# Performance work log

Hardware: AMD Instinct MI355X
Metric: run time of the kernel (lower is better)

Reference implementation:

```python
import jax, jax.numpy as jnp
import numpy as np

ALPHA = 0.2          # LeakyReLU negative slope
THRESHOLD = 0.5      # adjacency threshold
NEG_INF = -9e15      # same fill value as torch source


def setup_inputs() -> dict:
    key = jax.random.key(0)
    k_in, k_adj, k_W, k_a = jax.random.split(key, 4)
    B, N, C = 32, 1024, 64
    inp = jax.random.normal(k_in, (B, N, C), dtype=jnp.float32)
    adj = jax.random.uniform(k_adj, (N, N), dtype=jnp.float32)
    # xavier_uniform with gain=1.414 (as in torch init)
    gain = 1.414
    lim_W = gain * np.sqrt(6.0 / (C + C))
    W = jax.random.uniform(k_W, (C, C), dtype=jnp.float32, minval=-lim_W, maxval=lim_W)
    lim_a = gain * np.sqrt(6.0 / (2 * C + 1))
    a = jax.random.uniform(k_a, (2 * C, 1), dtype=jnp.float32, minval=-lim_a, maxval=lim_a)
    return {"input": inp, "adj": adj, "W": W, "a": a}


def reference(input, adj, W, a):
    # h: [B, N, C]
    h = jnp.matmul(input, W)
    C = W.shape[0]
    a_src = a[:C, 0]   # applied to h_i (row / query node)
    a_dst = a[C:, 0]   # applied to h_j (col / neighbor node)
    # Algebraic decomposition of a^T [h_i || h_j]: outer-sum of two [B,N] vectors.
    s_src = jnp.matmul(h, a_src)  # [B, N]
    s_dst = jnp.matmul(h, a_dst)  # [B, N]
    e = jax.nn.leaky_relu(s_src[:, :, None] + s_dst[:, None, :], negative_slope=ALPHA)  # [B,N,N]
    mask = adj > THRESHOLD  # [N, N], broadcast over batch
    attention = jax.nn.softmax(jnp.where(mask[None, :, :], e, NEG_INF), axis=2)
    h_prime = jnp.matmul(attention, h)  # [B, N, C]
    return jax.nn.elu(h_prime)
```

## Files before the change

kernel.cpp:

```cpp
#include <hip/hip_runtime.h>
#include <math.h>

#define ALPHA 0.2f

constexpr int B = 32, N = 1024, C = 64;

typedef __attribute__((ext_vector_type(8))) short short8;
typedef __attribute__((ext_vector_type(4))) float floatx4;

static __device__ __forceinline__ unsigned f32bf(float f) {
    unsigned u = __float_as_uint(f);
    return (u + 0x7FFFu + ((u >> 16) & 1u)) >> 16;
}

__global__ __launch_bounds__(256) void gat_mask(const float* __restrict__ adj,
                                                const float* __restrict__ Wm,
                                                const float* __restrict__ a,
                                                unsigned long long* __restrict__ mask64,
                                                float* __restrict__ wa)
{
    const int lane = threadIdx.x & 63;
    const int wave = threadIdx.x >> 6;
    const int id   = blockIdx.x * 4 + wave;
    const int i    = id >> 4;
    const int jc   = id & 15;
    const float av = adj[(size_t)i * N + jc * 64 + lane];
    const unsigned long long bal = __ballot(av > 0.5f);
    if (lane == 0) mask64[i * 16 + jc] = bal;

    if (blockIdx.x == 0 && wave == 0) {
        float accs = 0.f, accd = 0.f;
#pragma unroll
        for (int c4 = 0; c4 < 16; ++c4) {
            const float4 wv = *(const float4*)&Wm[lane * 64 + c4 * 4];
            const float4 as = *(const float4*)&a[c4 * 4];
            const float4 ad = *(const float4*)&a[64 + c4 * 4];
            accs = fmaf(wv.x, as.x, fmaf(wv.y, as.y, fmaf(wv.z, as.z, fmaf(wv.w, as.w, accs))));
            accd = fmaf(wv.x, ad.x, fmaf(wv.y, ad.y, fmaf(wv.z, ad.z, fmaf(wv.w, ad.w, accd))));
        }
        wa[lane] = accs;
        wa[64 + lane] = accd;
    }
}

__global__ __launch_bounds__(256) void gat_hs(const float* __restrict__ input,
                                              const float* __restrict__ Wm,
                                              const float* __restrict__ wa,
                                              unsigned short* __restrict__ hT,
                                              float* __restrict__ ssrc,
                                              float* __restrict__ sdst)
{
    __shared__ __align__(16) float ins[64 * 68];
    __shared__ __align__(16) unsigned short hsT[64 * 72];
    __shared__ float red_s[256], red_d[256];
    __shared__ float wa_l[128];

    const int tid  = threadIdx.x;
    const int lane = tid & 63;
    const int wave = tid >> 6;
    const int row0 = blockIdx.x * 64;
    const int b    = row0 >> 10;
    const int jb   = row0 & 1023;

    float wreg[64];
#pragma unroll
    for (int k = 0; k < 64; ++k) wreg[k] = Wm[k * 64 + lane];

    const float4* gin = (const float4*)(input + (size_t)row0 * 64);
#pragma unroll
    for (int s = 0; s < 4; ++s) {
        const int id = tid + 256 * s;
        *(float4*)&ins[(id >> 4) * 68 + (id & 15) * 4] = gin[id];
    }
    if (tid < 128) wa_l[tid] = wa[tid];
    __syncthreads();

    for (int r = 0; r < 16; ++r) {
        const int row = wave * 16 + r;
        float acc = 0.f;
#pragma unroll
        for (int k4 = 0; k4 < 16; ++k4) {
            const float4 iv = *(const float4*)&ins[row * 68 + k4 * 4];
            acc = fmaf(iv.x, wreg[k4 * 4 + 0], acc);
            acc = fmaf(iv.y, wreg[k4 * 4 + 1], acc);
            acc = fmaf(iv.z, wreg[k4 * 4 + 2], acc);
            acc = fmaf(iv.w, wreg[k4 * 4 + 3], acc);
        }
        hsT[lane * 72 + row] = (unsigned short)f32bf(acc);
    }

    {
        const int r = tid & 63, kq = tid >> 6;
        float as = 0.f, ad = 0.f;
#pragma unroll
        for (int t = 0; t < 4; ++t) {
            const float4 iv = *(const float4*)&ins[r * 68 + kq * 16 + t * 4];
            const float4 ws = *(const float4*)&wa_l[kq * 16 + t * 4];
            const float4 wd = *(const float4*)&wa_l[64 + kq * 16 + t * 4];
            as = fmaf(iv.x, ws.x, fmaf(iv.y, ws.y, fmaf(iv.z, ws.z, fmaf(iv.w, ws.w, as))));
            ad = fmaf(iv.x, wd.x, fmaf(iv.y, wd.y, fmaf(iv.z, wd.z, fmaf(iv.w, wd.w, ad))));
        }
        red_s[tid] = as;
        red_d[tid] = ad;
    }
    __syncthreads();

    if (tid < 64) {
        ssrc[row0 + tid] = red_s[tid] + red_s[tid + 64] + red_s[tid + 128] + red_s[tid + 192];
        sdst[row0 + tid] = red_d[tid] + red_d[tid + 64] + red_d[tid + 128] + red_d[tid + 192];
    }

    {
        const int c = tid >> 2, part = tid & 3;
        const short8 v0 = *(const short8*)&hsT[c * 72 + part * 16];
        const short8 v1 = *(const short8*)&hsT[c * 72 + part * 16 + 8];
        const size_t g = ((size_t)(b * 64 + c)) * 1024 + jb + part * 16;
        *(short8*)&hT[g] = v0;
        *(short8*)&hT[g + 8] = v1;
    }
}

__global__ __launch_bounds__(256) void gat_attn(const unsigned short* __restrict__ hTg,
                                                const float* __restrict__ ssrc,
                                                const float* __restrict__ sdst,
                                                const unsigned char* __restrict__ maskB,
                                                float* __restrict__ out)
{
    __shared__ __align__(16) unsigned short p_u[2][32 * 64];
    __shared__ float psum_s[32];

    const int tid  = threadIdx.x;
    const int lane = tid & 63;
    const int wave = tid >> 6;
    const int b    = blockIdx.x & 31;
    const int i0   = (blockIdx.x >> 5) * 32;

    const int ii = tid >> 3;
    const int jo = tid & 7;
    const float ssq = ssrc[b * N + i0 + ii];
    const float* __restrict__ sd = sdst + b * N;
    const unsigned char* __restrict__ mrow = maskB + (size_t)(i0 + ii) * 128;

    const int n16 = lane & 15;
    const int kq  = lane >> 4;
    const int cB  = wave * 16 + n16;
    const unsigned short* __restrict__ hTb = hTg + ((size_t)b * 64 + cB) * 1024;

    const int pwoff = ii * 64 + (jo ^ (ii & 7)) * 8;
    const int sw    = (n16 & 7);
    const int ra0   = n16 * 64;
    const int ra1   = (16 + n16) * 64;
    const int ch0   = ((0 * 4 + kq) ^ sw) * 8;
    const int ch1   = ((1 * 4 + kq) ^ sw) * 8;

    floatx4 acc0 = {0.f, 0.f, 0.f, 0.f};
    floatx4 acc1 = {0.f, 0.f, 0.f, 0.f};
    float psacc = 0.f;

    auto compute_p = [&](int jt) -> short8 {
        const float4 s0 = *(const float4*)&sd[jt * 64 + jo * 8];
        const float4 s1 = *(const float4*)&sd[jt * 64 + jo * 8 + 4];
        const unsigned mb = mrow[jt * 8 + jo];
        const float ev[8] = {s0.x, s0.y, s0.z, s0.w, s1.x, s1.y, s1.z, s1.w};
        short8 r;
        float loc = 0.f;
#pragma unroll
        for (int k = 0; k < 8; ++k) {
            float t = ssq + ev[k];
            t = t > 0.f ? t : ALPHA * t;
            const float p = ((mb >> k) & 1u) ? __expf(t) : 0.f;
            loc += p;
            r[k] = (short)f32bf(p);
        }
        psacc += loc;
        return r;
    };
    auto load_B = [&](int jt, int t) -> short8 {
        return *(const short8*)&hTb[jt * 64 + t * 32 + kq * 8];
    };

    short8 pk = compute_p(0);
    short8 b0 = load_B(0, 0);
    short8 b1 = load_B(0, 1);

    for (int jt = 0; jt < 16; ++jt) {
        unsigned short* pb = p_u[jt & 1];
        *(short8*)&pb[pwoff] = pk;
        __syncthreads();

        short8 nb0 = b0, nb1 = b1, npk = pk;
        if (jt < 15) {
            nb0 = load_B(jt + 1, 0);
            nb1 = load_B(jt + 1, 1);
            npk = compute_p(jt + 1);
        }

        const short8 a00 = *(const short8*)&pb[ra0 + ch0];
        const short8 a01 = *(const short8*)&pb[ra0 + ch1];
        const short8 a10 = *(const short8*)&pb[ra1 + ch0];
        const short8 a11 = *(const short8*)&pb[ra1 + ch1];
        acc0 = __builtin_amdgcn_mfma_f32_16x16x32_bf16(a00, b0, acc0, 0, 0, 0);
        acc0 = __builtin_amdgcn_mfma_f32_16x16x32_bf16(a01, b1, acc0, 0, 0, 0);
        acc1 = __builtin_amdgcn_mfma_f32_16x16x32_bf16(a10, b0, acc1, 0, 0, 0);
        acc1 = __builtin_amdgcn_mfma_f32_16x16x32_bf16(a11, b1, acc1, 0, 0, 0);

        b0 = nb0; b1 = nb1; pk = npk;
    }

#pragma unroll
    for (int off = 1; off < 8; off <<= 1) psacc += __shfl_xor(psacc, off, 64);
    if (jo == 0) psum_s[ii] = psacc;
    __syncthreads();

#pragma unroll
    for (int it = 0; it < 2; ++it) {
        const floatx4 acc = it ? acc1 : acc0;
#pragma unroll
        for (int r = 0; r < 4; ++r) {
            const int row = it * 16 + kq * 4 + r;
            const float hp = acc[r] / psum_s[row];
            const float o  = hp > 0.f ? hp : __expf(hp) - 1.f;
            out[((size_t)(b * N + i0 + row)) * 64 + cB] = o;
        }
    }
}

extern "C" void kernel_launch(void* const* d_in, const int* in_sizes, int n_in,
                              void* d_out, int out_size, void* d_ws, size_t ws_size,
                              hipStream_t stream) {
    const float* input = (const float*)d_in[0];
    const float* adj   = (const float*)d_in[1];
    const float* Wm    = (const float*)d_in[2];
    const float* a     = (const float*)d_in[3];
    float* out = (float*)d_out;

    char* ws = (char*)d_ws;
    unsigned short* hT = (unsigned short*)ws;
    float* ssrc = (float*)(ws + 4194304);
    float* sdst = (float*)(ws + 4194304 + 131072);
    unsigned long long* mask64 = (unsigned long long*)(ws + 4194304 + 2 * 131072);
    float* wa = (float*)(ws + 4194304 + 3 * 131072);

    gat_mask<<<N * N / 64 / 4, 256, 0, stream>>>(adj, Wm, a, mask64, wa);
    gat_hs<<<B * N / 64, 256, 0, stream>>>(input, Wm, wa, hT, ssrc, sdst);
    gat_attn<<<(N / 32) * B, 256, 0, stream>>>(hT, ssrc, sdst, (const unsigned char*)mask64, out);
}
```

Measured before the change: 105.4 us.

## Fuse mask and projection kernels, use MFMA for projection, stage attention tiles via LDS

```diff
diff --git a/kernel.cpp b/kernel.cpp
--- a/kernel.cpp
+++ b/kernel.cpp
@@ -2,6 +2,7 @@
 #include <math.h>
 
 #define ALPHA 0.2f
+#define LOG2E 1.4426950408889634f
 
 constexpr int B = 32, N = 1024, C = 64;
 
@@ -13,202 +14,208 @@
     return (u + 0x7FFFu + ((u >> 16) & 1u)) >> 16;
 }
 
-__global__ __launch_bounds__(256) void gat_mask(const float* __restrict__ adj,
-                                                const float* __restrict__ Wm,
-                                                const float* __restrict__ a,
-                                                unsigned long long* __restrict__ mask64,
-                                                float* __restrict__ wa)
+static __device__ __forceinline__ void async_copy16(void* lds_base, const void* g) {
+    __builtin_amdgcn_global_load_lds(
+        (const __attribute__((address_space(1))) unsigned int*)g,
+        (__attribute__((address_space(3))) unsigned int*)lds_base, 16, 0, 0);
+}
+
+__global__ __launch_bounds__(256) void gat_pre(
+    const float* __restrict__ input, const float* __restrict__ adj,
+    const float* __restrict__ Wm, const float* __restrict__ a,
+    unsigned short* __restrict__ hT, float* __restrict__ ssrc,
+    float* __restrict__ sdst, unsigned long long* __restrict__ mask64)
 {
-    const int lane = threadIdx.x & 63;
-    const int wave = threadIdx.x >> 6;
-    const int id   = blockIdx.x * 4 + wave;
-    const int i    = id >> 4;
-    const int jc   = id & 15;
-    const float av = adj[(size_t)i * N + jc * 64 + lane];
-    const unsigned long long bal = __ballot(av > 0.5f);
-    if (lane == 0) mask64[i * 16 + jc] = bal;
-
-    if (blockIdx.x == 0 && wave == 0) {
-        float accs = 0.f, accd = 0.f;
-#pragma unroll
-        for (int c4 = 0; c4 < 16; ++c4) {
-            const float4 wv = *(const float4*)&Wm[lane * 64 + c4 * 4];
-            const float4 as = *(const float4*)&a[c4 * 4];
-            const float4 ad = *(const float4*)&a[64 + c4 * 4];
-            accs = fmaf(wv.x, as.x, fmaf(wv.y, as.y, fmaf(wv.z, as.z, fmaf(wv.w, as.w, accs))));
-            accd = fmaf(wv.x, ad.x, fmaf(wv.y, ad.y, fmaf(wv.z, ad.z, fmaf(wv.w, ad.w, accd))));
-        }
-        wa[lane] = accs;
-        wa[64 + lane] = accd;
-    }
-}
-
-__global__ __launch_bounds__(256) void gat_hs(const float* __restrict__ input,
-                                              const float* __restrict__ Wm,
-                                              const float* __restrict__ wa,
-                                              unsigned short* __restrict__ hT,
-                                              float* __restrict__ ssrc,
-                                              float* __restrict__ sdst)
+    const int tid = threadIdx.x, lane = tid & 63, wave = tid >> 6;
+
+    if (blockIdx.x >= 1024) {
+        const int mb = blockIdx.x - 1024;
+#pragma unroll
+        for (int t = 0; t < 4; ++t) {
+            const int id = mb * 16 + wave * 4 + t;
+            const int i = id >> 4, jc = id & 15;
+            const float av = adj[(size_t)i * N + jc * 64 + lane];
+            const unsigned long long bal = __ballot(av > 0.5f);
+            if (lane == 0) mask64[i * 16 + jc] = bal;
+        }
+        return;
+    }
+
+    __shared__ __align__(16) float W_l[64 * 65];
+    __shared__ __align__(16) float a_l[128];
+    __shared__ float wa_l[128];
+
+    const int row0 = blockIdx.x * 32;
+    const int b = row0 >> 10;
+    const int jloc0 = row0 & 1023;
+    const int m = lane & 15, kq = lane >> 4;
+
+#pragma unroll
+    for (int t = 0; t < 4; ++t) {
+        const int t4 = tid + t * 256;
+        const int base = t4 * 4;
+        *(float4*)&W_l[(base >> 6) * 65 + (base & 63)] = ((const float4*)Wm)[t4];
+    }
+    if (tid < 32) ((float4*)a_l)[tid] = ((const float4*)a)[tid];
+
+    float af[2][2][8];
+#pragma unroll
+    for (int at = 0; at < 2; ++at)
+#pragma unroll
+        for (int kc = 0; kc < 2; ++kc) {
+            const float* src = &input[(size_t)(row0 + at * 16 + m) * 64 + kc * 32 + kq * 8];
+            const float4 v0 = *(const float4*)src;
+            const float4 v1 = *(const float4*)(src + 4);
+            af[at][kc][0] = v0.x; af[at][kc][1] = v0.y; af[at][kc][2] = v0.z; af[at][kc][3] = v0.w;
+            af[at][kc][4] = v1.x; af[at][kc][5] = v1.y; af[at][kc][6] = v1.z; af[at][kc][7] = v1.w;
+        }
+
+    __syncthreads();
+
+    if (wave < 2) {
+        const float* arow = a_l + wave * 64;
+        float acc = 0.f;
+        for (int t = 0; t < 64; ++t) {
+            const int c = (t + lane) & 63;
+            acc = fmaf(W_l[lane * 65 + c], arow[c], acc);
+        }
+        wa_l[wave * 64 + lane] = acc;
+    }
+
+    short8 bfr[2];
+#pragma unroll
+    for (int kc = 0; kc < 2; ++kc)
+#pragma unroll
+        for (int e = 0; e < 8; ++e)
+            bfr[kc][e] = (short)f32bf(W_l[(kc * 32 + kq * 8 + e) * 65 + wave * 16 + m]);
+
+    floatx4 acc[2] = {{0.f,0.f,0.f,0.f},{0.f,0.f,0.f,0.f}};
+#pragma unroll
+    for (int at = 0; at < 2; ++at) {
+        short8 afr0, afr1;
+#pragma unroll
+        for (int e = 0; e < 8; ++e) {
+            afr0[e] = (short)f32bf(af[at][0][e]);
+            afr1[e] = (short)f32bf(af[at][1][e]);
+        }
+        acc[at] = __builtin_amdgcn_mfma_f32_16x16x32_bf16(afr0, bfr[0], acc[at], 0, 0, 0);
+        acc[at] = __builtin_amdgcn_mfma_f32_16x16x32_bf16(afr1, bfr[1], acc[at], 0, 0, 0);
+    }
+
+    __syncthreads();
+
+#pragma unroll
+    for (int at = 0; at < 2; ++at) {
+        float vs = 0.f, vd = 0.f;
+#pragma unroll
+        for (int kc = 0; kc < 2; ++kc)
+#pragma unroll
+            for (int e = 0; e < 8; ++e) {
+                const float x = af[at][kc][e];
+                vs = fmaf(x, wa_l[kc * 32 + kq * 8 + e], vs);
+                vd = fmaf(x, wa_l[64 + kc * 32 + kq * 8 + e], vd);
+            }
+        vs += __shfl_xor(vs, 16, 64); vs += __shfl_xor(vs, 32, 64);
+        vd += __shfl_xor(vd, 16, 64); vd += __shfl_xor(vd, 32, 64);
+        if (wave == 0 && kq == 0) ssrc[row0 + at * 16 + m] = vs * LOG2E;
+        if (wave == 1 && kq == 0) sdst[row0 + at * 16 + m] = vd * LOG2E;
+    }
+
+#pragma unroll
+    for (int at = 0; at < 2; ++at) {
+        const uint2 v = {f32bf(acc[at][0]) | (f32bf(acc[at][1]) << 16),
+                         f32bf(acc[at][2]) | (f32bf(acc[at][3]) << 16)};
+        const size_t off = ((size_t)(b * 64 + wave * 16 + m)) * 1024 + jloc0 + at * 16 + kq * 4;
+        *(uint2*)&hT[off] = v;
+    }
+}
+
+__global__ __launch_bounds__(256) void gat_attn(
+    const unsigned short* __restrict__ hTg, const float* __restrict__ ssrc,
+    const float* __restrict__ sdst, const unsigned char* __restrict__ maskB,
+    float* __restrict__ out)
 {
-    __shared__ __align__(16) float ins[64 * 68];
-    __shared__ __align__(16) unsigned short hsT[64 * 72];
-    __shared__ float red_s[256], red_d[256];
-    __shared__ float wa_l[128];
-
-    const int tid  = threadIdx.x;
-    const int lane = tid & 63;
-    const int wave = tid >> 6;
-    const int row0 = blockIdx.x * 64;
-    const int b    = row0 >> 10;
-    const int jb   = row0 & 1023;
-
-    float wreg[64];
-#pragma unroll
-    for (int k = 0; k < 64; ++k) wreg[k] = Wm[k * 64 + lane];
-
-    const float4* gin = (const float4*)(input + (size_t)row0 * 64);
-#pragma unroll
-    for (int s = 0; s < 4; ++s) {
-        const int id = tid + 256 * s;
-        *(float4*)&ins[(id >> 4) * 68 + (id & 15) * 4] = gin[id];
-    }
-    if (tid < 128) wa_l[tid] = wa[tid];
-    __syncthreads();
-
-    for (int r = 0; r < 16; ++r) {
-        const int row = wave * 16 + r;
-        float acc = 0.f;
-#pragma unroll
-        for (int k4 = 0; k4 < 16; ++k4) {
-            const float4 iv = *(const float4*)&ins[row * 68 + k4 * 4];
-            acc = fmaf(iv.x, wreg[k4 * 4 + 0], acc);
-            acc = fmaf(iv.y, wreg[k4 * 4 + 1], acc);
-            acc = fmaf(iv.z, wreg[k4 * 4 + 2], acc);
-            acc = fmaf(iv.w, wreg[k4 * 4 + 3], acc);
-        }
-        hsT[lane * 72 + row] = (unsigned short)f32bf(acc);
-    }
-
-    {
-        const int r = tid & 63, kq = tid >> 6;
-        float as = 0.f, ad = 0.f;
-#pragma unroll
-        for (int t = 0; t < 4; ++t) {
-            const float4 iv = *(const float4*)&ins[r * 68 + kq * 16 + t * 4];
-            const float4 ws = *(const float4*)&wa_l[kq * 16 + t * 4];
-            const float4 wd = *(const float4*)&wa_l[64 + kq * 16 + t * 4];
-            as = fmaf(iv.x, ws.x, fmaf(iv.y, ws.y, fmaf(iv.z, ws.z, fmaf(iv.w, ws.w, as))));
-            ad = fmaf(iv.x, wd.x, fmaf(iv.y, wd.y, fmaf(iv.z, wd.z, fmaf(iv.w, wd.w, ad))));
-        }
-        red_s[tid] = as;
-        red_d[tid] = ad;
-    }
-    __syncthreads();
-
-    if (tid < 64) {
-        ssrc[row0 + tid] = red_s[tid] + red_s[tid + 64] + red_s[tid + 128] + red_s[tid + 192];
-        sdst[row0 + tid] = red_d[tid] + red_d[tid + 64] + red_d[tid + 128] + red_d[tid + 192];
-    }
-
-    {
-        const int c = tid >> 2, part = tid & 3;
-        const short8 v0 = *(const short8*)&hsT[c * 72 + part * 16];
-        const short8 v1 = *(const short8*)&hsT[c * 72 + part * 16 + 8];
-        const size_t g = ((size_t)(b * 64 + c)) * 1024 + jb + part * 16;
-        *(short8*)&hT[g] = v0;
-        *(short8*)&hT[g + 8] = v1;
-    }
-}
-
-__global__ __launch_bounds__(256) void gat_attn(const unsigned short* __restrict__ hTg,
-                                                const float* __restrict__ ssrc,
-                                                const float* __restrict__ sdst,
-                                                const unsigned char* __restrict__ maskB,
-                                                float* __restrict__ out)
-{
-    __shared__ __align__(16) unsigned short p_u[2][32 * 64];
+    __shared__ __align__(16) unsigned short h_u[64 * 64];
+    __shared__ __align__(16) unsigned short p_u[32 * 64];
+    __shared__ __align__(16) float sd_l[1024];
     __shared__ float psum_s[32];
 
-    const int tid  = threadIdx.x;
-    const int lane = tid & 63;
-    const int wave = tid >> 6;
-    const int b    = blockIdx.x & 31;
-    const int i0   = (blockIdx.x >> 5) * 32;
-
-    const int ii = tid >> 3;
-    const int jo = tid & 7;
+    const int tid = threadIdx.x, lane = tid & 63, wave = tid >> 6;
+    const int b = blockIdx.x & 31;
+    const int i0 = (blockIdx.x >> 5) * 32;
+
+    ((float4*)sd_l)[tid] = ((const float4*)(sdst + b * N))[tid];
+
+    const int ii = tid >> 3, jo = tid & 7;
     const float ssq = ssrc[b * N + i0 + ii];
-    const float* __restrict__ sd = sdst + b * N;
     const unsigned char* __restrict__ mrow = maskB + (size_t)(i0 + ii) * 128;
 
-    const int n16 = lane & 15;
-    const int kq  = lane >> 4;
-    const int cB  = wave * 16 + n16;
-    const unsigned short* __restrict__ hTb = hTg + ((size_t)b * 64 + cB) * 1024;
-
+    unsigned mreg[4];
+#pragma unroll
+    for (int q = 0; q < 4; ++q) {
+        unsigned v = 0;
+#pragma unroll
+        for (int t = 0; t < 4; ++t)
+            v |= (unsigned)mrow[(q * 4 + t) * 8 + jo] << (t * 8);
+        mreg[q] = v;
+    }
+
+    const int n16 = lane & 15, kq = lane >> 4;
+    const int cB = wave * 16 + n16;
+    const unsigned short* __restrict__ hTb = hTg + (size_t)b * 64 * 1024;
+
+    const int rr = lane >> 3;
+    const int sg = (lane & 7) ^ rr;
     const int pwoff = ii * 64 + (jo ^ (ii & 7)) * 8;
-    const int sw    = (n16 & 7);
-    const int ra0   = n16 * 64;
-    const int ra1   = (16 + n16) * 64;
-    const int ch0   = ((0 * 4 + kq) ^ sw) * 8;
-    const int ch1   = ((1 * 4 + kq) ^ sw) * 8;
-
-    floatx4 acc0 = {0.f, 0.f, 0.f, 0.f};
-    floatx4 acc1 = {0.f, 0.f, 0.f, 0.f};
+
+    floatx4 acc0 = {0.f,0.f,0.f,0.f}, acc1 = {0.f,0.f,0.f,0.f};
     float psacc = 0.f;
 
-    auto compute_p = [&](int jt) -> short8 {
-        const float4 s0 = *(const float4*)&sd[jt * 64 + jo * 8];
-        const float4 s1 = *(const float4*)&sd[jt * 64 + jo * 8 + 4];
-        const unsigned mb = mrow[jt * 8 + jo];
+#pragma unroll
+    for (int jt = 0; jt < 16; ++jt) {
+        __syncthreads();
+
+#pragma unroll
+        for (int s = 0; s < 2; ++s) {
+            const int r8 = wave * 16 + s * 8;
+            async_copy16(&h_u[r8 * 64],
+                         hTb + (size_t)(r8 + rr) * 1024 + jt * 64 + sg * 8);
+        }
+
+        const unsigned mb = (mreg[jt >> 2] >> ((jt & 3) * 8)) & 0xffu;
+        const float4 s0 = *(const float4*)&sd_l[jt * 64 + jo * 8];
+        const float4 s1 = *(const float4*)&sd_l[jt * 64 + jo * 8 + 4];
         const float ev[8] = {s0.x, s0.y, s0.z, s0.w, s1.x, s1.y, s1.z, s1.w};
-        short8 r;
+        short8 pk;
         float loc = 0.f;
 #pragma unroll
         for (int k = 0; k < 8; ++k) {
             float t = ssq + ev[k];
             t = t > 0.f ? t : ALPHA * t;
-            const float p = ((mb >> k) & 1u) ? __expf(t) : 0.f;
+            const float p = ((mb >> k) & 1u) ? exp2f(t) : 0.f;
             loc += p;
-            r[k] = (short)f32bf(p);
+            pk[k] = (short)f32bf(p);
         }
         psacc += loc;
-        return r;
-    };
-    auto load_B = [&](int jt, int t) -> short8 {
-        return *(const short8*)&hTb[jt * 64 + t * 32 + kq * 8];
-    };
-
-    short8 pk = compute_p(0);
-    short8 b0 = load_B(0, 0);
-    short8 b1 = load_B(0, 1);
-
-    for (int jt = 0; jt < 16; ++jt) {
-        unsigned short* pb = p_u[jt & 1];
-        *(short8*)&pb[pwoff] = pk;
+        *(short8*)&p_u[pwoff] = pk;
+
         __syncthreads();
 
-        short8 nb0 = b0, nb1 = b1, npk = pk;
-        if (jt < 15) {
-            nb0 = load_B(jt + 1, 0);
-            nb1 = load_B(jt + 1, 1);
-            npk = compute_p(jt + 1);
-        }
-
-        const short8 a00 = *(const short8*)&pb[ra0 + ch0];
-        const short8 a01 = *(const short8*)&pb[ra0 + ch1];
-        const short8 a10 = *(const short8*)&pb[ra1 + ch0];
-        const short8 a11 = *(const short8*)&pb[ra1 + ch1];
-        acc0 = __builtin_amdgcn_mfma_f32_16x16x32_bf16(a00, b0, acc0, 0, 0, 0);
-        acc0 = __builtin_amdgcn_mfma_f32_16x16x32_bf16(a01, b1, acc0, 0, 0, 0);
-        acc1 = __builtin_amdgcn_mfma_f32_16x16x32_bf16(a10, b0, acc1, 0, 0, 0);
-        acc1 = __builtin_amdgcn_mfma_f32_16x16x32_bf16(a11, b1, acc1, 0, 0, 0);
-
-        b0 = nb0; b1 = nb1; pk = npk;
-    }
-
-#pragma unroll
-    for (int off = 1; off < 8; off <<= 1) psacc += __shfl_xor(psacc, off, 64);
+#pragma unroll
+        for (int kc = 0; kc < 2; ++kc) {
+            const int ch = ((kc * 4 + kq) ^ (cB & 7)) * 8;
+            const int ca = ((kc * 4 + kq) ^ (n16 & 7)) * 8;
+            const short8 bfr = *(const short8*)&h_u[cB * 64 + ch];
+            const short8 a0  = *(const short8*)&p_u[n16 * 64 + ca];
+            const short8 a1  = *(const short8*)&p_u[(16 + n16) * 64 + ca];
+            acc0 = __builtin_amdgcn_mfma_f32_16x16x32_bf16(a0, bfr, acc0, 0, 0, 0);
+            acc1 = __builtin_amdgcn_mfma_f32_16x16x32_bf16(a1, bfr, acc1, 0, 0, 0);
+        }
+    }
+
+    psacc += __shfl_xor(psacc, 1, 64);
+    psacc += __shfl_xor(psacc, 2, 64);
+    psacc += __shfl_xor(psacc, 4, 64);
     if (jo == 0) psum_s[ii] = psacc;
     __syncthreads();
 
@@ -219,7 +226,7 @@
         for (int r = 0; r < 4; ++r) {
             const int row = it * 16 + kq * 4 + r;
             const float hp = acc[r] / psum_s[row];
-            const float o  = hp > 0.f ? hp : __expf(hp) - 1.f;
+            const float o = hp > 0.f ? hp : __expf(hp) - 1.f;
             out[((size_t)(b * N + i0 + row)) * 64 + cB] = o;
         }
     }
@@ -239,9 +246,7 @@
     float* ssrc = (float*)(ws + 4194304);
     float* sdst = (float*)(ws + 4194304 + 131072);
     unsigned long long* mask64 = (unsigned long long*)(ws + 4194304 + 2 * 131072);
-    float* wa = (float*)(ws + 4194304 + 3 * 131072);
-
-    gat_mask<<<N * N / 64 / 4, 256, 0, stream>>>(adj, Wm, a, mask64, wa);
-    gat_hs<<<B * N / 64, 256, 0, stream>>>(input, Wm, wa, hT, ssrc, sdst);
-    gat_attn<<<(N / 32) * B, 256, 0, stream>>>(hT, ssrc, sdst, (const unsigned char*)mask64, out);
-}
+
+    gat_pre<<<2048, 256, 0, stream>>>(input, adj, Wm, a, hT, ssrc, sdst, mask64);
+    gat_attn<<<1024, 256, 0, stream>>>(hT, ssrc, sdst, (const unsigned char*)mask64, out);
+}
```

Result: no change. 104.0 us (-1.4%).
